# Performance work log

Measured on AMD Instinct MI355X. Metric: run time of the kernel, lower is better.

## Reference

```python
import jax, jax.numpy as jnp
import numpy as np

DIM = 128
NUM_HEADS = 4
HEAD_DIM = DIM // NUM_HEADS
WS = 8            # window height/width
SHIFT = 4
N_CAND = 4        # candidates per spatial position
H_RES, W_RES = 64, 128
M = WS * WS       # tokens per window spatially
L = M * N_CAND    # window sequence length
NW = (H_RES // WS) * (W_RES // WS)
B = 1
B_ = NW * B
NEG_INF = -1e9  # finite stand-in for -inf; softmax result identical within fp tolerance


def _rel_position_index():
    ch = np.arange(WS); cw = np.arange(WS)
    coords = np.stack(np.meshgrid(ch, cw, indexing='ij')).reshape(2, -1)  # [2, M]
    rel = (coords[:, :, None] - coords[:, None, :]).transpose(1, 2, 0)    # [M, M, 2]
    rel = rel + np.array([WS - 1, WS - 1])
    rel[..., 0] *= 2 * WS - 1
    return rel.sum(-1).astype(np.int32)  # [M, M] in [0, (2WS-1)^2)


def _window_attn_mask():
    # block message passing between same spatial position's candidates (except self)
    idx = np.repeat(np.arange(M), N_CAND).astype(np.float64)  # [L]
    m = idx[:, None] - idx[None, :]
    mask = np.where(m == 0, NEG_INF, 0.0)
    mask[np.arange(L), np.arange(L)] = 0.0
    return mask  # [L, L]


def _shift_window_attn_mask():
    img = np.zeros((H_RES, W_RES))
    cnt = 0
    for hs in (slice(0, -WS), slice(-WS, -SHIFT), slice(-SHIFT, None)):
        for ws in (slice(0, -WS), slice(-WS, -SHIFT), slice(-SHIFT, None)):
            img[hs, ws] = cnt
            cnt += 1
    mw = img.reshape(H_RES // WS, WS, W_RES // WS, WS).transpose(0, 2, 1, 3).reshape(-1, M)  # [nW, M]
    am = mw[:, None, :] - mw[:, :, None]           # [nW, M, M]
    am = np.where(am != 0, NEG_INF, 0.0)
    am = np.repeat(np.repeat(am, N_CAND, axis=1), N_CAND, axis=2)  # [nW, L, L]
    return am + _window_attn_mask()[None]


def setup_inputs() -> dict:
    key = jax.random.key(0)
    ks = jax.random.split(key, 6)
    x = jax.random.normal(ks[0], (B_, L, DIM), dtype=jnp.float32)
    qkv_w = jax.random.normal(ks[1], (3 * DIM, DIM), dtype=jnp.float32) * 0.02
    qkv_b = jnp.zeros((3 * DIM,), dtype=jnp.float32)
    rpe_table = jax.random.normal(ks[2], ((2 * WS - 1) ** 2, 3 * DIM), dtype=jnp.float32) * 0.02
    proj_w = jax.random.normal(ks[3], (DIM, DIM), dtype=jnp.float32) * 0.02
    proj_b = jnp.zeros((DIM,), dtype=jnp.float32)
    attn_mask = jnp.asarray(_shift_window_attn_mask(), dtype=jnp.float32)
    rel_idx = jnp.asarray(_rel_position_index())
    return {"x": x, "qkv_w": qkv_w, "qkv_b": qkv_b, "rpe_table": rpe_table,
            "proj_w": proj_w, "proj_b": proj_b, "attn_mask": attn_mask, "rel_idx": rel_idx}


def reference(x, qkv_w, qkv_b, rpe_table, proj_w, proj_b, attn_mask, rel_idx):
    b_, l, _ = x.shape
    h, hd = NUM_HEADS, HEAD_DIM
    scale = hd ** -0.5
    # QKV projection -> [B_, h, L, hd] each
    qkv = (x @ qkv_w.T + qkv_b).reshape(b_, l, 3, h, hd).transpose(2, 0, 3, 1, 4)
    q, k, v = qkv[0], qkv[1], qkv[2]
    # relative-position encodings gathered per (i, j) pair, expanded over candidates
    m = rel_idx.shape[0]
    n = l // m
    rpe = rpe_table[rel_idx.reshape(-1)].reshape(m, m, h, 3 * hd)
    rpe = jnp.repeat(jnp.repeat(rpe, n, axis=0), n, axis=1)  # [L, L, h, 3*hd]
    q_rpe, k_rpe, v_rpe = jnp.split(rpe, 3, axis=-1)
    q = q * scale
    q_rpe = q_rpe * scale
    qk = jnp.einsum('bhic,bhjc->bhij', q, k)
    qr = jnp.einsum('bhic,ijhc->bhij', q, k_rpe)
    kr = jnp.einsum('bhjc,ijhc->bhij', k, q_rpe)
    attn = qk + qr + kr  # [B_, h, L, L]
    nw = attn_mask.shape[0]
    attn = attn.reshape(b_ // nw, nw, h, l, l) + attn_mask[None, :, None]
    attn = attn.reshape(b_, h, l, l)
    attn = jax.nn.softmax(attn.astype(jnp.float32), axis=-1).astype(x.dtype)
    out = jnp.einsum('bhij,bhjc->bhic', attn, v) + jnp.einsum('bhij,ijhc->bhic', attn, v_rpe)
    out = out.transpose(0, 2, 1, 3).reshape(b_, l, DIM)
    return out @ proj_w.T + proj_b
```

## Files before the change

kernel.cpp:

```cpp
#include <hip/hip_runtime.h>
#include <math.h>

constexpr int HD    = 32;
constexpr int LW    = 256;
constexpr int NWIN  = 128;
constexpr int ROWS  = NWIN * LW;
constexpr int QKVC  = 384;
constexpr float SCALE = 0.17677669529663687f;

__device__ inline float dot4(const float4 a, const float4 b) {
  return a.x * b.x + a.y * b.y + a.z * b.z + a.w * b.w;
}

__global__ __launch_bounds__(256) void rpe_gather_kernel(
    const float* __restrict__ tab, const int* __restrict__ rel_idx,
    float* __restrict__ out)
{
  int gid = blockIdx.x * 256 + threadIdx.x;
  int s   = gid % 96;
  int hp  = gid / 96;
  int p   = hp & 4095;
  int h   = hp >> 12;
  float v = tab[(size_t)rel_idx[p] * 384 + h * 96 + s];
  if (s < 32) v *= SCALE;
  out[gid] = v;
}

template <int N, int K>
__global__ __launch_bounds__(256) void gemm_nt_bias_v3(
    const float* __restrict__ A, const float* __restrict__ W,
    const float* __restrict__ bias, float* __restrict__ C)
{
  constexpr int BK  = 8;
  constexpr int NS  = K / BK;
  constexpr int LDP = 144;
  __shared__ float As[2][BK][LDP];
  __shared__ float Ws[2][BK][LDP];

  const int tid  = threadIdx.x;
  const int tx   = tid & 15;
  const int ty   = tid >> 4;
  const int srow = tid >> 1;
  const int skk  = (tid & 1) << 2;
  const int sphys = srow + ((srow >> 5) << 2);

  const float* Ag = A + ((size_t)blockIdx.x * 128 + srow) * K + skk;
  const float* Wg = W + ((size_t)blockIdx.y * 128 + srow) * K + skk;

  float4 ra = *(const float4*)(Ag);
  float4 rw = *(const float4*)(Wg);
  As[0][skk + 0][sphys] = ra.x; As[0][skk + 1][sphys] = ra.y;
  As[0][skk + 2][sphys] = ra.z; As[0][skk + 3][sphys] = ra.w;
  Ws[0][skk + 0][sphys] = rw.x; Ws[0][skk + 1][sphys] = rw.y;
  Ws[0][skk + 2][sphys] = rw.z; Ws[0][skk + 3][sphys] = rw.w;
  __syncthreads();

  const int mA = ty * 8; const int pA = mA + ((mA >> 5) << 2);
  const int mB = tx * 8; const int pB = mB + ((mB >> 5) << 2);

  float acc[8][8] = {};

  for (int s = 0; s < NS; ++s) {
    const int cur = s & 1;
    if (s + 1 < NS) {
      const int k0 = (s + 1) * BK;
      ra = *(const float4*)(Ag + k0);
      rw = *(const float4*)(Wg + k0);
    }
#pragma unroll
    for (int k = 0; k < BK; ++k) {
      float4 a0 = *(const float4*)&As[cur][k][pA];
      float4 a1 = *(const float4*)&As[cur][k][pA + 4];
      float4 b0 = *(const float4*)&Ws[cur][k][pB];
      float4 b1 = *(const float4*)&Ws[cur][k][pB + 4];
      float av[8] = {a0.x, a0.y, a0.z, a0.w, a1.x, a1.y, a1.z, a1.w};
      float bv[8] = {b0.x, b0.y, b0.z, b0.w, b1.x, b1.y, b1.z, b1.w};
#pragma unroll
      for (int i = 0; i < 8; ++i)
#pragma unroll
        for (int j = 0; j < 8; ++j)
          acc[i][j] += av[i] * bv[j];
    }
    if (s + 1 < NS) {
      const int nxt = (s + 1) & 1;
      As[nxt][skk + 0][sphys] = ra.x; As[nxt][skk + 1][sphys] = ra.y;
      As[nxt][skk + 2][sphys] = ra.z; As[nxt][skk + 3][sphys] = ra.w;
      Ws[nxt][skk + 0][sphys] = rw.x; Ws[nxt][skk + 1][sphys] = rw.y;
      Ws[nxt][skk + 2][sphys] = rw.z; Ws[nxt][skk + 3][sphys] = rw.w;
      __syncthreads();
    }
  }

  const int crow = blockIdx.x * 128 + ty * 8;
  const int ccol = blockIdx.y * 128 + tx * 8;
  float4 bb0 = *(const float4*)(bias + ccol);
  float4 bb1 = *(const float4*)(bias + ccol + 4);
#pragma unroll
  for (int i = 0; i < 8; ++i) {
    float4 r0, r1;
    r0.x = acc[i][0] + bb0.x; r0.y = acc[i][1] + bb0.y;
    r0.z = acc[i][2] + bb0.z; r0.w = acc[i][3] + bb0.w;
    r1.x = acc[i][4] + bb1.x; r1.y = acc[i][5] + bb1.y;
    r1.z = acc[i][6] + bb1.z; r1.w = acc[i][7] + bb1.w;
    *(float4*)(C + (size_t)(crow + i) * N + ccol)     = r0;
    *(float4*)(C + (size_t)(crow + i) * N + ccol + 4) = r1;
  }
}

__global__ __launch_bounds__(256) void attn_kernel(
    const float* __restrict__ qkv, const float* __restrict__ rpeg,
    const float* __restrict__ mask, float* __restrict__ out)
{
  __shared__ float kvs[2 * LW * HD];
  const int b = blockIdx.x;
  const int h = blockIdx.y;
  const int tid = threadIdx.x;
  const size_t rowbase = (size_t)b * LW;

  for (int it = 0; it < 8; ++it) {
    int f = tid + 256 * it;
    int j = f >> 3, d4 = f & 7;
    const float* src = qkv + (rowbase + j) * QKVC + h * HD + d4 * 4;
    *(float4*)(&kvs[j * HD + d4 * 4])            = *(const float4*)(src + 128);
    *(float4*)(&kvs[LW * HD + j * HD + d4 * 4])  = *(const float4*)(src + 256);
  }
  __syncthreads();

  const int i  = tid;
  const int i4 = i >> 2;
  float4 q[8];
  {
    const float4* qr = (const float4*)(qkv + (rowbase + i) * QKVC + h * HD);
#pragma unroll
    for (int d = 0; d < 8; ++d) {
      float4 t = qr[d];
      q[d] = make_float4(t.x * SCALE, t.y * SCALE, t.z * SCALE, t.w * SCALE);
    }
  }
  const float4* rp4base =
      (const float4*)(rpeg + ((size_t)h * 4096 + (size_t)i4 * 64) * 96);
  const float* mrow = mask + ((size_t)b * LW + i) * LW;

  float4 acc[8];
#pragma unroll
  for (int d = 0; d < 8; ++d) acc[d] = make_float4(0.f, 0.f, 0.f, 0.f);
  float m_run = -INFINITY, l_run = 0.f;

  for (int j4 = 0; j4 < 64; ++j4) {
    const float4* rp = rp4base + j4 * 24;
    float4 u[8];
    float c0 = 0.f;
#pragma unroll
    for (int d = 0; d < 8; ++d) {
      float4 sq = rp[d];
      float4 kr = rp[8 + d];
      u[d] = make_float4(q[d].x + sq.x, q[d].y + sq.y,
                         q[d].z + sq.z, q[d].w + sq.w);
      c0 += dot4(q[d], kr);
    }
    float4 mv = *(const float4*)(mrow + j4 * 4);
    float mvals[4] = {mv.x, mv.y, mv.z, mv.w};
    float pool = 0.f;
#pragma unroll
    for (int jc = 0; jc < 4; ++jc) {
      const int j = j4 * 4 + jc;
      const float4* kj = (const float4*)(&kvs[j * HD]);
      float s = c0 + mvals[jc];
#pragma unroll
      for (int d = 0; d < 8; ++d) s += dot4(u[d], kj[d]);
      if (s > m_run) {
        float r = __expf(m_run - s);
        m_run = s;
        l_run *= r; pool *= r;
#pragma unroll
        for (int d = 0; d < 8; ++d) {
          acc[d].x *= r; acc[d].y *= r; acc[d].z *= r; acc[d].w *= r;
        }
      }
      float p = __expf(s - m_run);
      l_run += p; pool += p;
      const float4* vj = (const float4*)(&kvs[LW * HD + j * HD]);
#pragma unroll
      for (int d = 0; d < 8; ++d) {
        acc[d].x += p * vj[d].x; acc[d].y += p * vj[d].y;
        acc[d].z += p * vj[d].z; acc[d].w += p * vj[d].w;
      }
    }
#pragma unroll
    for (int d = 0; d < 8; ++d) {
      float4 vr = rp[16 + d];
      acc[d].x += pool * vr.x; acc[d].y += pool * vr.y;
      acc[d].z += pool * vr.z; acc[d].w += pool * vr.w;
    }
  }
  float inv = 1.f / l_run;
  float4* orow = (float4*)(out + (rowbase + i) * (4 * HD) + h * HD);
#pragma unroll
  for (int d = 0; d < 8; ++d)
    orow[d] = make_float4(acc[d].x * inv, acc[d].y * inv,
                          acc[d].z * inv, acc[d].w * inv);
}

extern "C" void kernel_launch(void* const* d_in, const int* in_sizes, int n_in,
                              void* d_out, int out_size, void* d_ws, size_t ws_size,
                              hipStream_t stream) {
  (void)in_sizes; (void)n_in; (void)out_size; (void)ws_size;
  const float* x         = (const float*)d_in[0];
  const float* qkv_w     = (const float*)d_in[1];
  const float* qkv_b     = (const float*)d_in[2];
  const float* rpe_table = (const float*)d_in[3];
  const float* proj_w    = (const float*)d_in[4];
  const float* proj_b    = (const float*)d_in[5];
  const float* attn_mask = (const float*)d_in[6];
  const int*   rel_idx   = (const int*)d_in[7];
  float* out = (float*)d_out;

  float* qkvbuf = (float*)d_ws;
  float* rpeg   = qkvbuf + (size_t)ROWS * QKVC;
  float* attnb  = rpeg + (size_t)4 * 4096 * 96;

  hipLaunchKernelGGL(rpe_gather_kernel, dim3(6144), dim3(256), 0, stream,
                     rpe_table, rel_idx, rpeg);
  hipLaunchKernelGGL((gemm_nt_bias_v3<QKVC, 128>), dim3(ROWS / 128, QKVC / 128),
                     dim3(256), 0, stream, x, qkv_w, qkv_b, qkvbuf);
  hipLaunchKernelGGL(attn_kernel, dim3(NWIN, 4), dim3(256), 0, stream,
                     qkvbuf, rpeg, attn_mask, attnb);
  hipLaunchKernelGGL((gemm_nt_bias_v3<128, 128>), dim3(ROWS / 128, 1),
                     dim3(256), 0, stream, attnb, proj_w, proj_b, out);
}
```

Before: 326.3 us.

## Split attention key range across two thread groups and skip fully masked key blocks

The attention kernel now runs 512 threads per block. Each query row is handled by two threads, each covering half of the key range with its own online-softmax state. The two partial states are merged through shared memory at the end. Key blocks of four that the mask fully blocks for every lane in the wave are skipped with a wave vote. The aim is more parallelism and occupancy on a grid of only 512 blocks, at the cost of extra synchronisation, a merge step and more register pressure under the new launch bounds.

```diff
diff --git a/kernel.cpp b/kernel.cpp
--- a/kernel.cpp
+++ b/kernel.cpp
@@ -107,7 +107,7 @@
   }
 }
 
-__global__ __launch_bounds__(256) void attn_kernel(
+__global__ __launch_bounds__(512, 4) void attn_kernel(
     const float* __restrict__ qkv, const float* __restrict__ rpeg,
     const float* __restrict__ mask, float* __restrict__ out)
 {
@@ -115,10 +115,13 @@
   const int b = blockIdx.x;
   const int h = blockIdx.y;
   const int tid = threadIdx.x;
+  const int grp = tid >> 8;
+  const int i   = tid & 255;
+  const int i4  = i >> 2;
   const size_t rowbase = (size_t)b * LW;
 
-  for (int it = 0; it < 8; ++it) {
-    int f = tid + 256 * it;
+  for (int it = 0; it < 4; ++it) {
+    int f = tid + 512 * it;
     int j = f >> 3, d4 = f & 7;
     const float* src = qkv + (rowbase + j) * QKVC + h * HD + d4 * 4;
     *(float4*)(&kvs[j * HD + d4 * 4])            = *(const float4*)(src + 128);
@@ -126,8 +129,6 @@
   }
   __syncthreads();
 
-  const int i  = tid;
-  const int i4 = i >> 2;
   float4 q[8];
   {
     const float4* qr = (const float4*)(qkv + (rowbase + i) * QKVC + h * HD);
@@ -146,7 +147,12 @@
   for (int d = 0; d < 8; ++d) acc[d] = make_float4(0.f, 0.f, 0.f, 0.f);
   float m_run = -INFINITY, l_run = 0.f;
 
-  for (int j4 = 0; j4 < 64; ++j4) {
+  const int j4e = grp * 32 + 32;
+  for (int j4 = grp * 32; j4 < j4e; ++j4) {
+    float4 mv = *(const float4*)(mrow + j4 * 4);
+    float mm = fmaxf(fmaxf(mv.x, mv.y), fmaxf(mv.z, mv.w));
+    if (__all(mm < -1e8f)) continue;
+
     const float4* rp = rp4base + j4 * 24;
     float4 u[8];
     float c0 = 0.f;
@@ -158,7 +164,6 @@
                          q[d].z + sq.z, q[d].w + sq.w);
       c0 += dot4(q[d], kr);
     }
-    float4 mv = *(const float4*)(mrow + j4 * 4);
     float mvals[4] = {mv.x, mv.y, mv.z, mv.w};
     float pool = 0.f;
 #pragma unroll
@@ -193,12 +198,36 @@
       acc[d].z += pool * vr.z; acc[d].w += pool * vr.w;
     }
   }
-  float inv = 1.f / l_run;
-  float4* orow = (float4*)(out + (rowbase + i) * (4 * HD) + h * HD);
-#pragma unroll
-  for (int d = 0; d < 8; ++d)
-    orow[d] = make_float4(acc[d].x * inv, acc[d].y * inv,
-                          acc[d].z * inv, acc[d].w * inv);
+
+  __syncthreads();
+  constexpr int CST = 37;
+  float* row = kvs + i * CST;
+  if (grp == 1) {
+    row[0] = m_run; row[1] = l_run;
+#pragma unroll
+    for (int d = 0; d < 8; ++d) {
+      row[2 + 4 * d + 0] = acc[d].x; row[2 + 4 * d + 1] = acc[d].y;
+      row[2 + 4 * d + 2] = acc[d].z; row[2 + 4 * d + 3] = acc[d].w;
+    }
+  }
+  __syncthreads();
+  if (grp == 0) {
+    float m1 = row[0], l1 = row[1];
+    float M  = fmaxf(m_run, m1);
+    float r0 = __expf(m_run - M);
+    float r1 = __expf(m1 - M);
+    float inv = 1.f / (l_run * r0 + l1 * r1);
+    float4* orow = (float4*)(out + (rowbase + i) * (4 * HD) + h * HD);
+#pragma unroll
+    for (int d = 0; d < 8; ++d) {
+      float ax = row[2 + 4 * d + 0], ay = row[2 + 4 * d + 1];
+      float az = row[2 + 4 * d + 2], aw = row[2 + 4 * d + 3];
+      orow[d] = make_float4((acc[d].x * r0 + ax * r1) * inv,
+                            (acc[d].y * r0 + ay * r1) * inv,
+                            (acc[d].z * r0 + az * r1) * inv,
+                            (acc[d].w * r0 + aw * r1) * inv);
+    }
+  }
 }
 
 extern "C" void kernel_launch(void* const* d_in, const int* in_sizes, int n_in,
@@ -223,7 +252,7 @@
                      rpe_table, rel_idx, rpeg);
   hipLaunchKernelGGL((gemm_nt_bias_v3<QKVC, 128>), dim3(ROWS / 128, QKVC / 128),
                      dim3(256), 0, stream, x, qkv_w, qkv_b, qkvbuf);
-  hipLaunchKernelGGL(attn_kernel, dim3(NWIN, 4), dim3(256), 0, stream,
+  hipLaunchKernelGGL(attn_kernel, dim3(NWIN, 4), dim3(512), 0, stream,
                      qkvbuf, rpeg, attn_mask, attnb);
   hipLaunchKernelGGL((gemm_nt_bias_v3<128, 128>), dim3(ROWS / 128, 1),
                      dim3(256), 0, stream, attnb, proj_w, proj_b, out);
```

Measured after the change: 356.0 us. 1.09x slower.

## Split attention keys across two blocks with flash-style merge and mask skipping

Applied to the files above, without the earlier changes.

The attention kernel now splits the 256 keys of each window into two halves on a third grid dimension, so twice as many blocks run and each needs half the shared memory. Each half writes its running max, sum and unnormalized accumulator to a workspace, and a new merge kernel combines them. Inside the loop it also skips groups of four keys when every lane's mask is fully negative, and does the online softmax once per group of four instead of once per key. The cost is an extra partial buffer in global memory and an extra kernel launch, and the skip test depends on the mask values being large negative numbers.

```diff
diff --git a/kernel.cpp b/kernel.cpp
--- a/kernel.cpp
+++ b/kernel.cpp
@@ -107,22 +107,24 @@
   }
 }
 
-__global__ __launch_bounds__(256) void attn_kernel(
+__global__ __launch_bounds__(256, 4) void attn_kernel(
     const float* __restrict__ qkv, const float* __restrict__ rpeg,
-    const float* __restrict__ mask, float* __restrict__ out)
-{
-  __shared__ float kvs[2 * LW * HD];
-  const int b = blockIdx.x;
-  const int h = blockIdx.y;
+    const float* __restrict__ mask, float* __restrict__ part)
+{
+  __shared__ float kvs[2 * 128 * HD];
+  const int b   = blockIdx.x;
+  const int h   = blockIdx.y;
+  const int z   = blockIdx.z;
   const int tid = threadIdx.x;
   const size_t rowbase = (size_t)b * LW;
-
-  for (int it = 0; it < 8; ++it) {
+  const int j0 = z * 128;
+
+  for (int it = 0; it < 4; ++it) {
     int f = tid + 256 * it;
     int j = f >> 3, d4 = f & 7;
-    const float* src = qkv + (rowbase + j) * QKVC + h * HD + d4 * 4;
+    const float* src = qkv + (rowbase + j0 + j) * QKVC + h * HD + d4 * 4;
     *(float4*)(&kvs[j * HD + d4 * 4])            = *(const float4*)(src + 128);
-    *(float4*)(&kvs[LW * HD + j * HD + d4 * 4])  = *(const float4*)(src + 256);
+    *(float4*)(&kvs[128 * HD + j * HD + d4 * 4]) = *(const float4*)(src + 256);
   }
   __syncthreads();
 
@@ -146,59 +148,96 @@
   for (int d = 0; d < 8; ++d) acc[d] = make_float4(0.f, 0.f, 0.f, 0.f);
   float m_run = -INFINITY, l_run = 0.f;
 
-  for (int j4 = 0; j4 < 64; ++j4) {
-    const float4* rp = rp4base + j4 * 24;
-    float4 u[8];
+  for (int jl = 0; jl < 32; ++jl) {
+    const int j4 = z * 32 + jl;
+    float4 mv = *(const float4*)(mrow + j4 * 4);
+    float mm4 = fmaxf(fmaxf(mv.x, mv.y), fmaxf(mv.z, mv.w));
+    if (__all(mm4 < -1e8f)) continue;
+
+    const float4* rp = rp4base + (size_t)j4 * 24;
+    const float4* kb = (const float4*)(&kvs[jl * 4 * HD]);
+    float s0 = mv.x, s1 = mv.y, s2 = mv.z, s3 = mv.w;
     float c0 = 0.f;
 #pragma unroll
     for (int d = 0; d < 8; ++d) {
+      float4 qd = q[d];
       float4 sq = rp[d];
-      float4 kr = rp[8 + d];
-      u[d] = make_float4(q[d].x + sq.x, q[d].y + sq.y,
-                         q[d].z + sq.z, q[d].w + sq.w);
-      c0 += dot4(q[d], kr);
-    }
-    float4 mv = *(const float4*)(mrow + j4 * 4);
-    float mvals[4] = {mv.x, mv.y, mv.z, mv.w};
-    float pool = 0.f;
-#pragma unroll
-    for (int jc = 0; jc < 4; ++jc) {
-      const int j = j4 * 4 + jc;
-      const float4* kj = (const float4*)(&kvs[j * HD]);
-      float s = c0 + mvals[jc];
-#pragma unroll
-      for (int d = 0; d < 8; ++d) s += dot4(u[d], kj[d]);
-      if (s > m_run) {
-        float r = __expf(m_run - s);
-        m_run = s;
-        l_run *= r; pool *= r;
-#pragma unroll
-        for (int d = 0; d < 8; ++d) {
-          acc[d].x *= r; acc[d].y *= r; acc[d].z *= r; acc[d].w *= r;
-        }
+      float4 u  = make_float4(qd.x + sq.x, qd.y + sq.y,
+                              qd.z + sq.z, qd.w + sq.w);
+      c0 += dot4(qd, rp[8 + d]);
+      s0 += dot4(u, kb[d]);
+      s1 += dot4(u, kb[8 + d]);
+      s2 += dot4(u, kb[16 + d]);
+      s3 += dot4(u, kb[24 + d]);
+    }
+    s0 += c0; s1 += c0; s2 += c0; s3 += c0;
+
+    float mm = fmaxf(fmaxf(s0, s1), fmaxf(s2, s3));
+    if (mm > m_run) {
+      float r = __expf(m_run - mm);
+      l_run *= r;
+#pragma unroll
+      for (int d = 0; d < 8; ++d) {
+        acc[d].x *= r; acc[d].y *= r; acc[d].z *= r; acc[d].w *= r;
       }
-      float p = __expf(s - m_run);
-      l_run += p; pool += p;
-      const float4* vj = (const float4*)(&kvs[LW * HD + j * HD]);
-#pragma unroll
-      for (int d = 0; d < 8; ++d) {
-        acc[d].x += p * vj[d].x; acc[d].y += p * vj[d].y;
-        acc[d].z += p * vj[d].z; acc[d].w += p * vj[d].w;
-      }
-    }
+      m_run = mm;
+    }
+    float p0 = __expf(s0 - m_run), p1 = __expf(s1 - m_run);
+    float p2 = __expf(s2 - m_run), p3 = __expf(s3 - m_run);
+    float pool = p0 + p1 + p2 + p3;
+    l_run += pool;
+    const float4* vb = (const float4*)(&kvs[128 * HD + jl * 4 * HD]);
 #pragma unroll
     for (int d = 0; d < 8; ++d) {
+      float4 a  = acc[d];
+      float4 v0 = vb[d],      v1 = vb[8 + d];
+      float4 v2 = vb[16 + d], v3 = vb[24 + d];
       float4 vr = rp[16 + d];
-      acc[d].x += pool * vr.x; acc[d].y += pool * vr.y;
-      acc[d].z += pool * vr.z; acc[d].w += pool * vr.w;
-    }
-  }
-  float inv = 1.f / l_run;
-  float4* orow = (float4*)(out + (rowbase + i) * (4 * HD) + h * HD);
-#pragma unroll
-  for (int d = 0; d < 8; ++d)
-    orow[d] = make_float4(acc[d].x * inv, acc[d].y * inv,
-                          acc[d].z * inv, acc[d].w * inv);
+      a.x += p0 * v0.x + p1 * v1.x + p2 * v2.x + p3 * v3.x + pool * vr.x;
+      a.y += p0 * v0.y + p1 * v1.y + p2 * v2.y + p3 * v3.y + pool * vr.y;
+      a.z += p0 * v0.z + p1 * v1.z + p2 * v2.z + p3 * v3.z + pool * vr.z;
+      a.w += p0 * v0.w + p1 * v1.w + p2 * v2.w + p3 * v3.w + pool * vr.w;
+      acc[d] = a;
+    }
+  }
+
+  float* pb = part + ((size_t)(z * 512 + b * 4 + h) * 34) * 256 + i;
+  pb[0]   = m_run;
+  pb[256] = l_run;
+#pragma unroll
+  for (int d = 0; d < 8; ++d) {
+    pb[(2 + 4 * d + 0) * 256] = acc[d].x;
+    pb[(2 + 4 * d + 1) * 256] = acc[d].y;
+    pb[(2 + 4 * d + 2) * 256] = acc[d].z;
+    pb[(2 + 4 * d + 3) * 256] = acc[d].w;
+  }
+}
+
+__global__ __launch_bounds__(256) void merge_kernel(
+    const float* __restrict__ part, float* __restrict__ out)
+{
+  const int bh = blockIdx.x;
+  const int i  = threadIdx.x;
+  const int b  = bh >> 2, h = bh & 3;
+  const float* p0 = part + (size_t)bh * 34 * 256 + i;
+  const float* p1 = p0 + (size_t)512 * 34 * 256;
+  float m0 = p0[0], l0 = p0[256];
+  float m1 = p1[0], l1 = p1[256];
+  float M  = fmaxf(m0, m1);
+  float r0 = __expf(m0 - M);
+  float r1 = __expf(m1 - M);
+  float inv = 1.f / (l0 * r0 + l1 * r1);
+  r0 *= inv; r1 *= inv;
+  float* orow = out + ((size_t)b * LW + i) * 128 + h * HD;
+#pragma unroll
+  for (int d = 0; d < 8; ++d) {
+    float4 o;
+    o.x = p0[(2 + 4 * d + 0) * 256] * r0 + p1[(2 + 4 * d + 0) * 256] * r1;
+    o.y = p0[(2 + 4 * d + 1) * 256] * r0 + p1[(2 + 4 * d + 1) * 256] * r1;
+    o.z = p0[(2 + 4 * d + 2) * 256] * r0 + p1[(2 + 4 * d + 2) * 256] * r1;
+    o.w = p0[(2 + 4 * d + 3) * 256] * r0 + p1[(2 + 4 * d + 3) * 256] * r1;
+    *(float4*)(orow + 4 * d) = o;
+  }
 }
 
 extern "C" void kernel_launch(void* const* d_in, const int* in_sizes, int n_in,
@@ -218,13 +257,16 @@
   float* qkvbuf = (float*)d_ws;
   float* rpeg   = qkvbuf + (size_t)ROWS * QKVC;
   float* attnb  = rpeg + (size_t)4 * 4096 * 96;
+  float* part   = attnb + (size_t)ROWS * 128;
 
   hipLaunchKernelGGL(rpe_gather_kernel, dim3(6144), dim3(256), 0, stream,
                      rpe_table, rel_idx, rpeg);
   hipLaunchKernelGGL((gemm_nt_bias_v3<QKVC, 128>), dim3(ROWS / 128, QKVC / 128),
                      dim3(256), 0, stream, x, qkv_w, qkv_b, qkvbuf);
-  hipLaunchKernelGGL(attn_kernel, dim3(NWIN, 4), dim3(256), 0, stream,
-                     qkvbuf, rpeg, attn_mask, attnb);
+  hipLaunchKernelGGL(attn_kernel, dim3(NWIN, 4, 2), dim3(256), 0, stream,
+                     qkvbuf, rpeg, attn_mask, part);
+  hipLaunchKernelGGL(merge_kernel, dim3(512), dim3(256), 0, stream,
+                     part, attnb);
   hipLaunchKernelGGL((gemm_nt_bias_v3<128, 128>), dim3(ROWS / 128, 1),
                      dim3(256), 0, stream, attnb, proj_w, proj_b, out);
 }
```

After: 441.6 us. +35.3%, slower.

## Precompute RPE score terms in separate kernels and skip fully masked blocks

Applied to the files above, without the earlier changes.

Adds two kernels that precompute the q·k_rpe term (c0) and the k·q_rpe term (t) per window, head and position pair, writing them to workspace buffers. The attention kernel then reads these instead of recomputing them. It processes four keys at a time with a single max-rescale per group, and skips a key group when every lane in the wavefront sees it fully masked. This cuts the inner-loop FLOPs and rescale branches, at the cost of about 67 MB of extra global traffic and two extra launches with only 256 blocks each.

```diff
diff --git a/kernel.cpp b/kernel.cpp
--- a/kernel.cpp
+++ b/kernel.cpp
@@ -107,9 +107,92 @@
   }
 }
 
+__global__ __launch_bounds__(256) void c0_kernel(
+    const float* __restrict__ qkv, const float* __restrict__ rpeg,
+    float* __restrict__ c0L)
+{
+  __shared__ float krs[64 * 32];
+  const int i4  = blockIdx.x;
+  const int h   = blockIdx.y;
+  const int tid = threadIdx.x;
+  for (int g = tid; g < 512; g += 256) {
+    int j4 = g >> 3, c4 = g & 7;
+    const float* src = rpeg + ((size_t)h * 4096 + i4 * 64 + j4) * 96 + 32 + c4 * 4;
+    *(float4*)(&krs[j4 * 32 + c4 * 4]) = *(const float4*)src;
+  }
+  __syncthreads();
+
+  const int b0 = tid >> 2;
+  const int ir = tid & 3;
+  const int i  = i4 * 4 + ir;
+  float4 q0[8], q1[8];
+  {
+    const float4* qr0 = (const float4*)(qkv + ((size_t)b0 * 256 + i) * QKVC + h * HD);
+    const float4* qr1 = (const float4*)(qkv + ((size_t)(b0 + 64) * 256 + i) * QKVC + h * HD);
+#pragma unroll
+    for (int d = 0; d < 8; ++d) { q0[d] = qr0[d]; q1[d] = qr1[d]; }
+  }
+  float* o0 = c0L + ((size_t)(b0 * 4 + h) * 64) * 256 + i;
+  float* o1 = c0L + ((size_t)((b0 + 64) * 4 + h) * 64) * 256 + i;
+  for (int j4 = 0; j4 < 64; ++j4) {
+    const float4* kr = (const float4*)(&krs[j4 * 32]);
+    float d0 = 0.f, d1 = 0.f;
+#pragma unroll
+    for (int d = 0; d < 8; ++d) {
+      float4 k = kr[d];
+      d0 += dot4(q0[d], k);
+      d1 += dot4(q1[d], k);
+    }
+    o0[j4 * 256] = d0 * SCALE;
+    o1[j4 * 256] = d1 * SCALE;
+  }
+}
+
+__global__ __launch_bounds__(256) void t_kernel(
+    const float* __restrict__ qkv, const float* __restrict__ rpeg,
+    float* __restrict__ tL)
+{
+  __shared__ float sqs[64 * 32];
+  const int j4  = blockIdx.x;
+  const int h   = blockIdx.y;
+  const int tid = threadIdx.x;
+  for (int g = tid; g < 512; g += 256) {
+    int i4 = g >> 3, c4 = g & 7;
+    const float* src = rpeg + ((size_t)h * 4096 + i4 * 64 + j4) * 96 + c4 * 4;
+    *(float4*)(&sqs[i4 * 32 + c4 * 4]) = *(const float4*)src;
+  }
+  __syncthreads();
+
+  const int b0 = tid >> 2;
+  const int jc = tid & 3;
+  const int j  = j4 * 4 + jc;
+  float4 k0[8], k1[8];
+  {
+    const float4* kr0 = (const float4*)(qkv + ((size_t)b0 * 256 + j) * QKVC + 128 + h * HD);
+    const float4* kr1 = (const float4*)(qkv + ((size_t)(b0 + 64) * 256 + j) * QKVC + 128 + h * HD);
+#pragma unroll
+    for (int d = 0; d < 8; ++d) { k0[d] = kr0[d]; k1[d] = kr1[d]; }
+  }
+  float* o0 = tL + ((size_t)(b0 * 4 + h) * 64) * 256 + j;
+  float* o1 = tL + ((size_t)((b0 + 64) * 4 + h) * 64) * 256 + j;
+  for (int i4 = 0; i4 < 64; ++i4) {
+    const float4* sq = (const float4*)(&sqs[i4 * 32]);
+    float d0 = 0.f, d1 = 0.f;
+#pragma unroll
+    for (int d = 0; d < 8; ++d) {
+      float4 s = sq[d];
+      d0 += dot4(k0[d], s);
+      d1 += dot4(k1[d], s);
+    }
+    o0[i4 * 256] = d0;
+    o1[i4 * 256] = d1;
+  }
+}
+
 __global__ __launch_bounds__(256) void attn_kernel(
     const float* __restrict__ qkv, const float* __restrict__ rpeg,
-    const float* __restrict__ mask, float* __restrict__ out)
+    const float* __restrict__ mask, const float* __restrict__ c0L,
+    const float* __restrict__ tL, float* __restrict__ out)
 {
   __shared__ float kvs[2 * LW * HD];
   const int b = blockIdx.x;
@@ -140,6 +223,8 @@
   const float4* rp4base =
       (const float4*)(rpeg + ((size_t)h * 4096 + (size_t)i4 * 64) * 96);
   const float* mrow = mask + ((size_t)b * LW + i) * LW;
+  const float* c0p  = c0L + ((size_t)(b * 4 + h) * 64) * 256 + i;
+  const float* tp   = tL  + (((size_t)(b * 4 + h) * 64 + i4)) * 256;
 
   float4 acc[8];
 #pragma unroll
@@ -147,52 +232,56 @@
   float m_run = -INFINITY, l_run = 0.f;
 
   for (int j4 = 0; j4 < 64; ++j4) {
-    const float4* rp = rp4base + j4 * 24;
-    float4 u[8];
-    float c0 = 0.f;
-#pragma unroll
-    for (int d = 0; d < 8; ++d) {
-      float4 sq = rp[d];
-      float4 kr = rp[8 + d];
-      u[d] = make_float4(q[d].x + sq.x, q[d].y + sq.y,
-                         q[d].z + sq.z, q[d].w + sq.w);
-      c0 += dot4(q[d], kr);
-    }
     float4 mv = *(const float4*)(mrow + j4 * 4);
-    float mvals[4] = {mv.x, mv.y, mv.z, mv.w};
-    float pool = 0.f;
-#pragma unroll
-    for (int jc = 0; jc < 4; ++jc) {
-      const int j = j4 * 4 + jc;
-      const float4* kj = (const float4*)(&kvs[j * HD]);
-      float s = c0 + mvals[jc];
-#pragma unroll
-      for (int d = 0; d < 8; ++d) s += dot4(u[d], kj[d]);
-      if (s > m_run) {
-        float r = __expf(m_run - s);
-        m_run = s;
-        l_run *= r; pool *= r;
-#pragma unroll
-        for (int d = 0; d < 8; ++d) {
-          acc[d].x *= r; acc[d].y *= r; acc[d].z *= r; acc[d].w *= r;
-        }
+    float mm4 = fmaxf(fmaxf(mv.x, mv.y), fmaxf(mv.z, mv.w));
+    if (__all(mm4 < -1e8f)) continue;
+
+    float  c0 = c0p[j4 * 256];
+    float4 tv = *(const float4*)(tp + j4 * 4);
+    const float4* kb = (const float4*)(&kvs[j4 * 4 * HD]);
+    float s0 = mv.x + c0 + tv.x;
+    float s1 = mv.y + c0 + tv.y;
+    float s2 = mv.z + c0 + tv.z;
+    float s3 = mv.w + c0 + tv.w;
+#pragma unroll
+    for (int d = 0; d < 8; ++d) {
+      float4 qd = q[d];
+      s0 += dot4(qd, kb[d]);
+      s1 += dot4(qd, kb[8 + d]);
+      s2 += dot4(qd, kb[16 + d]);
+      s3 += dot4(qd, kb[24 + d]);
+    }
+
+    float mm = fmaxf(fmaxf(s0, s1), fmaxf(s2, s3));
+    if (mm > m_run) {
+      float r = __expf(m_run - mm);
+      l_run *= r;
+#pragma unroll
+      for (int d = 0; d < 8; ++d) {
+        acc[d].x *= r; acc[d].y *= r; acc[d].z *= r; acc[d].w *= r;
       }
-      float p = __expf(s - m_run);
-      l_run += p; pool += p;
-      const float4* vj = (const float4*)(&kvs[LW * HD + j * HD]);
-#pragma unroll
-      for (int d = 0; d < 8; ++d) {
-        acc[d].x += p * vj[d].x; acc[d].y += p * vj[d].y;
-        acc[d].z += p * vj[d].z; acc[d].w += p * vj[d].w;
-      }
-    }
-#pragma unroll
-    for (int d = 0; d < 8; ++d) {
+      m_run = mm;
+    }
+    float p0 = __expf(s0 - m_run), p1 = __expf(s1 - m_run);
+    float p2 = __expf(s2 - m_run), p3 = __expf(s3 - m_run);
+    float pool = p0 + p1 + p2 + p3;
+    l_run += pool;
+    const float4* rp = rp4base + (size_t)j4 * 24;
+    const float4* vb = (const float4*)(&kvs[LW * HD + j4 * 4 * HD]);
+#pragma unroll
+    for (int d = 0; d < 8; ++d) {
+      float4 a  = acc[d];
+      float4 v0 = vb[d],      v1 = vb[8 + d];
+      float4 v2 = vb[16 + d], v3 = vb[24 + d];
       float4 vr = rp[16 + d];
-      acc[d].x += pool * vr.x; acc[d].y += pool * vr.y;
-      acc[d].z += pool * vr.z; acc[d].w += pool * vr.w;
-    }
-  }
+      a.x += p0 * v0.x + p1 * v1.x + p2 * v2.x + p3 * v3.x + pool * vr.x;
+      a.y += p0 * v0.y + p1 * v1.y + p2 * v2.y + p3 * v3.y + pool * vr.y;
+      a.z += p0 * v0.z + p1 * v1.z + p2 * v2.z + p3 * v3.z + pool * vr.z;
+      a.w += p0 * v0.w + p1 * v1.w + p2 * v2.w + p3 * v3.w + pool * vr.w;
+      acc[d] = a;
+    }
+  }
+
   float inv = 1.f / l_run;
   float4* orow = (float4*)(out + (rowbase + i) * (4 * HD) + h * HD);
 #pragma unroll
@@ -218,13 +307,19 @@
   float* qkvbuf = (float*)d_ws;
   float* rpeg   = qkvbuf + (size_t)ROWS * QKVC;
   float* attnb  = rpeg + (size_t)4 * 4096 * 96;
+  float* c0L    = attnb + (size_t)ROWS * 128;
+  float* tL     = c0L + (size_t)512 * 64 * 256;
 
   hipLaunchKernelGGL(rpe_gather_kernel, dim3(6144), dim3(256), 0, stream,
                      rpe_table, rel_idx, rpeg);
   hipLaunchKernelGGL((gemm_nt_bias_v3<QKVC, 128>), dim3(ROWS / 128, QKVC / 128),
                      dim3(256), 0, stream, x, qkv_w, qkv_b, qkvbuf);
+  hipLaunchKernelGGL(c0_kernel, dim3(64, 4), dim3(256), 0, stream,
+                     qkvbuf, rpeg, c0L);
+  hipLaunchKernelGGL(t_kernel, dim3(64, 4), dim3(256), 0, stream,
+                     qkvbuf, rpeg, tL);
   hipLaunchKernelGGL(attn_kernel, dim3(NWIN, 4), dim3(256), 0, stream,
-                     qkvbuf, rpeg, attn_mask, attnb);
+                     qkvbuf, rpeg, attn_mask, c0L, tL, attnb);
   hipLaunchKernelGGL((gemm_nt_bias_v3<128, 128>), dim3(ROWS / 128, 1),
                      dim3(256), 0, stream, attnb, proj_w, proj_b, out);
 }
```

After: 375.6 us. 15.1% more time.
